# Performance work log

Measured on AMD Instinct MI355X. Metric: run time of the kernel, lower is better.

## Reference

```python
import jax, jax.numpy as jnp
import numpy as np

N_NODES = 100000
N_EDGES = 1600000
N_GRAPHS = 512
HIDDEN = 128
N_LAYERS = 3


def setup_inputs() -> dict:
    key = jax.random.key(0)
    ks = jax.random.split(key, 16)
    X = jax.random.normal(ks[0], (N_NODES, HIDDEN), dtype=jnp.float32)
    edge_index = jax.random.randint(ks[1], (2, N_EDGES), 0, N_NODES, dtype=jnp.int64)
    batch = jnp.sort(jax.random.randint(ks[2], (N_NODES,), 0, N_GRAPHS, dtype=jnp.int64))
    s = 1.0 / np.sqrt(HIDDEN)
    mlp_w1 = jax.random.normal(ks[3], (N_LAYERS, HIDDEN, HIDDEN), dtype=jnp.float32) * s
    mlp_b1 = jnp.zeros((N_LAYERS, HIDDEN), dtype=jnp.float32)
    mlp_w2 = jax.random.normal(ks[4], (N_LAYERS, HIDDEN, HIDDEN), dtype=jnp.float32) * s
    mlp_b2 = jnp.zeros((N_LAYERS, HIDDEN), dtype=jnp.float32)
    cls_w1 = jax.random.normal(ks[5], (HIDDEN * N_LAYERS, HIDDEN), dtype=jnp.float32) / np.sqrt(HIDDEN * N_LAYERS)
    cls_b1 = jnp.zeros((HIDDEN,), dtype=jnp.float32)
    cls_w2 = jax.random.normal(ks[6], (HIDDEN, HIDDEN), dtype=jnp.float32) * s
    cls_b2 = jnp.zeros((HIDDEN,), dtype=jnp.float32)
    cls_w3 = jax.random.normal(ks[7], (HIDDEN, 1), dtype=jnp.float32) * s
    cls_b3 = jnp.zeros((1,), dtype=jnp.float32)
    return {"X": X, "edge_index": edge_index, "batch": batch,
            "mlp_w1": mlp_w1, "mlp_b1": mlp_b1, "mlp_w2": mlp_w2, "mlp_b2": mlp_b2,
            "cls_w1": cls_w1, "cls_b1": cls_b1, "cls_w2": cls_w2, "cls_b2": cls_b2,
            "cls_w3": cls_w3, "cls_b3": cls_b3}


def reference(X, edge_index, batch, mlp_w1, mlp_b1, mlp_w2, mlp_b2,
              cls_w1, cls_b1, cls_w2, cls_b2, cls_w3, cls_b3):
    src, dst = edge_index[0], edge_index[1]
    xs = []
    for l in range(N_LAYERS):
        # GIN aggregation: sum_{j in N(i)} x_j ; eps = 0 so add self feature
        agg = jax.ops.segment_sum(X[src], dst, num_segments=N_NODES)  # [N, H]
        z = X + agg
        # 2-layer MLP update
        h = jax.nn.relu(z @ mlp_w1[l] + mlp_b1[l])
        h = h @ mlp_w2[l] + mlp_b2[l]
        # dropout is identity in eval; then relu
        X = jax.nn.relu(h)
        # global sum pooling per graph
        xs.append(jax.ops.segment_sum(X, batch, num_segments=N_GRAPHS))  # [G, H]
    h = jnp.concatenate(xs, axis=-1)  # JK 'cat' -> [G, H*L]
    h = jax.nn.relu(h @ cls_w1 + cls_b1)
    h = jax.nn.relu(h @ cls_w2 + cls_b2)
    logits = h @ cls_w3 + cls_b3  # [G, 1]
    return logits
```

## Files before the change

### kernel.cpp

```cpp
#include <hip/hip_runtime.h>
#include <hip/hip_fp16.h>
#include <cstddef>
#include <cstdint>

#define N_NODES   100000
#define N_EDGES   1600000
#define N_GRAPHS  512
#define HIDDEN    128
#define N_LAYERS  3

#define N_WIN        400
#define WIN_NODES    (N_NODES / N_WIN)
#define PLACE_BLOCKS 128
#define PCHUNK       (N_EDGES / PLACE_BLOCKS)

#define F2H_BLOCKS   ((N_NODES * HIDDEN / 8) / 256)
#define WCONV_BLOCKS (N_LAYERS * 2 * 16)
#define GB_BLOCKS    2
#define PREP_BLOCKS  (F2H_BLOCKS + WCONV_BLOCKS + GB_BLOCKS)

typedef _Float16 half8  __attribute__((ext_vector_type(8)));
typedef _Float16 half4v __attribute__((ext_vector_type(4)));
typedef _Float16 half2v __attribute__((ext_vector_type(2)));
typedef float    float8 __attribute__((ext_vector_type(8)));
typedef float    floatx4 __attribute__((ext_vector_type(4)));
typedef float    floatx2 __attribute__((ext_vector_type(2)));

__global__ __launch_bounds__(256) void win_count_kernel(const int* __restrict__ dst,
                                                        int* __restrict__ counts) {
    __shared__ int cs[N_WIN];
    for (int i = threadIdx.x; i < N_WIN; i += 256) cs[i] = 0;
    __syncthreads();
    const int4* d4 = (const int4*)(dst + blockIdx.x * PCHUNK);
    for (int i = threadIdx.x; i < PCHUNK / 4; i += 256) {
        int4 d = d4[i];
        atomicAdd(&cs[d.x / WIN_NODES], 1);
        atomicAdd(&cs[d.y / WIN_NODES], 1);
        atomicAdd(&cs[d.z / WIN_NODES], 1);
        atomicAdd(&cs[d.w / WIN_NODES], 1);
    }
    __syncthreads();
    for (int i = threadIdx.x; i < N_WIN; i += 256)
        counts[blockIdx.x * N_WIN + i] = cs[i];
}

__global__ __launch_bounds__(128) void win_scan1_kernel(const int* __restrict__ counts,
                                                        int* __restrict__ offsets,
                                                        int* __restrict__ colsum) {
    __shared__ int tmp[128];
    const int w = blockIdx.x;
    const int t = threadIdx.x;
    tmp[t] = counts[t * N_WIN + w];
    __syncthreads();
#pragma unroll
    for (int off = 1; off < 128; off <<= 1) {
        int u = (t >= off) ? tmp[t - off] : 0;
        __syncthreads();
        tmp[t] += u;
        __syncthreads();
    }
    offsets[t * N_WIN + w] = (t == 0) ? 0 : tmp[t - 1];
    if (t == 127) colsum[w] = tmp[127];
}

__global__ __launch_bounds__(512) void win_place_kernel(const int* __restrict__ src,
                                                        const int* __restrict__ dst,
                                                        const int* __restrict__ offsets,
                                                        const int* __restrict__ colsum,
                                                        int2* __restrict__ wedge) {
    __shared__ int ws[512];
    __shared__ int off[N_WIN];
    const int t = threadIdx.x;
    ws[t] = (t < N_WIN) ? colsum[t] : 0;
    __syncthreads();
#pragma unroll
    for (int o = 1; o < 512; o <<= 1) {
        int u = (t >= o) ? ws[t - o] : 0;
        __syncthreads();
        ws[t] += u;
        __syncthreads();
    }
    if (t < N_WIN) off[t] = offsets[blockIdx.x * N_WIN + t] + ((t == 0) ? 0 : ws[t - 1]);
    __syncthreads();
    const int4* d4 = (const int4*)(dst + blockIdx.x * PCHUNK);
    const int4* s4 = (const int4*)(src + blockIdx.x * PCHUNK);
    for (int i = t; i < PCHUNK / 4; i += 512) {
        int4 d = d4[i];
        int4 s = s4[i];
        int p0 = atomicAdd(&off[d.x / WIN_NODES], 1); wedge[p0] = make_int2(d.x, s.x);
        int p1 = atomicAdd(&off[d.y / WIN_NODES], 1); wedge[p1] = make_int2(d.y, s.y);
        int p2 = atomicAdd(&off[d.z / WIN_NODES], 1); wedge[p2] = make_int2(d.z, s.z);
        int p3 = atomicAdd(&off[d.w / WIN_NODES], 1); wedge[p3] = make_int2(d.w, s.w);
    }
}

__global__ __launch_bounds__(512) void win_csr_kernel(const int2* __restrict__ wedge,
                                                      const int* __restrict__ colsum,
                                                      int* __restrict__ row_ptr,
                                                      int* __restrict__ csr_src) {
    __shared__ int ws[512];
    __shared__ int cnt[WIN_NODES];
    __shared__ int bb[2];
    const int w = blockIdx.x, n0 = w * WIN_NODES, t = threadIdx.x;
    ws[t] = (t < N_WIN) ? colsum[t] : 0;
    __syncthreads();
#pragma unroll
    for (int o = 1; o < 512; o <<= 1) {
        int u = (t >= o) ? ws[t - o] : 0;
        __syncthreads();
        ws[t] += u;
        __syncthreads();
    }
    if (t == 0) { bb[0] = (w > 0) ? ws[w - 1] : 0; bb[1] = ws[w]; }
    if (w == N_WIN - 1 && t == 0) row_ptr[N_NODES] = ws[N_WIN - 1];
    for (int i = t; i < WIN_NODES; i += 512) cnt[i] = 0;
    __syncthreads();
    const int b0 = bb[0], b1 = bb[1];
    for (int e = b0 + t; e < b1; e += 512)
        atomicAdd(&cnt[wedge[e].x - n0], 1);
    __syncthreads();
    ws[t] = (t < WIN_NODES) ? cnt[t] : 0;
    __syncthreads();
#pragma unroll
    for (int o = 1; o < 512; o <<= 1) {
        int u = (t >= o) ? ws[t - o] : 0;
        __syncthreads();
        ws[t] += u;
        __syncthreads();
    }
    const int excl = (t == 0) ? 0 : ws[t - 1];
    if (t < WIN_NODES) {
        row_ptr[n0 + t] = b0 + excl;
        cnt[t] = b0 + excl;
    }
    __syncthreads();
    for (int e = b0 + t; e < b1; e += 512) {
        int2 ed = wedge[e];
        int p = atomicAdd(&cnt[ed.x - n0], 1);
        csr_src[p] = ed.y;
    }
}

__global__ __launch_bounds__(256) void prep_kernel(const float* __restrict__ X,
                                                   __half* __restrict__ hA,
                                                   unsigned char* __restrict__ outq,
                                                   const float* __restrict__ w1,
                                                   const float* __restrict__ w2,
                                                   __half* __restrict__ wt1,
                                                   __half* __restrict__ wt2,
                                                   const int* __restrict__ batch,
                                                   int* __restrict__ gstart) {
    __shared__ float tile[32][33];
    const int b = blockIdx.x;
    if (b < F2H_BLOCKS) {
        int t = b * 256 + threadIdx.x;
        const float4* in4 = (const float4*)X;
        float4 a = in4[t * 2 + 0];
        float4 c = in4[t * 2 + 1];
        __half2* o2 = (__half2*)hA;
        o2[t * 4 + 0] = __floats2half2_rn(a.x, a.y);
        o2[t * 4 + 1] = __floats2half2_rn(a.z, a.w);
        o2[t * 4 + 2] = __floats2half2_rn(c.x, c.y);
        o2[t * 4 + 3] = __floats2half2_rn(c.z, c.w);
        unsigned r0 = 0, r1 = 0;
        r0 = __builtin_amdgcn_cvt_pk_fp8_f32(a.x, a.y, r0, false);
        r0 = __builtin_amdgcn_cvt_pk_fp8_f32(a.z, a.w, r0, true);
        r1 = __builtin_amdgcn_cvt_pk_fp8_f32(c.x, c.y, r1, false);
        r1 = __builtin_amdgcn_cvt_pk_fp8_f32(c.z, c.w, r1, true);
        ((uint2*)outq)[t] = make_uint2(r0, r1);
    } else if (b < F2H_BLOCKS + WCONV_BLOCKS) {
        const int bb = b - F2H_BLOCKS;
        const int mat = bb & 1;
        const int tt = (bb >> 1) & 15;
        const int l  = bb >> 5;
        const int ti = (tt >> 2) * 32, tj = (tt & 3) * 32;
        const float* W = (mat ? w2 : w1) + (size_t)l * HIDDEN * HIDDEN;
        __half* WT = (mat ? wt2 : wt1) + (size_t)l * HIDDEN * HIDDEN;
        const int r = threadIdx.x >> 5;
        const int c = threadIdx.x & 31;
#pragma unroll
        for (int rr = 0; rr < 4; ++rr)
            tile[r + 8 * rr][c] = W[(size_t)(ti + r + 8 * rr) * HIDDEN + tj + c];
        __syncthreads();
#pragma unroll
        for (int rr = 0; rr < 4; ++rr)
            WT[(size_t)(tj + r + 8 * rr) * HIDDEN + ti + c] =
                __float2half(tile[c][r + 8 * rr]);
    } else {
        const int g = (b - F2H_BLOCKS - WCONV_BLOCKS) * 256 + threadIdx.x;
        if (g < N_GRAPHS) {
            int lo = 0, hi = N_NODES;
            while (lo < hi) {
                int mid = (lo + hi) >> 1;
                if (batch[mid] < g) lo = mid + 1; else hi = mid;
            }
            gstart[g] = lo;
        }
        if (g == 0) gstart[N_GRAPHS] = N_NODES;
    }
}

__device__ __forceinline__ void acc_fp8x16(float* acc, uint4 v) {
    floatx2 f;
    f = __builtin_amdgcn_cvt_pk_f32_fp8(v.x, false); acc[0] += f.x;  acc[1] += f.y;
    f = __builtin_amdgcn_cvt_pk_f32_fp8(v.x, true);  acc[2] += f.x;  acc[3] += f.y;
    f = __builtin_amdgcn_cvt_pk_f32_fp8(v.y, false); acc[4] += f.x;  acc[5] += f.y;
    f = __builtin_amdgcn_cvt_pk_f32_fp8(v.y, true);  acc[6] += f.x;  acc[7] += f.y;
    f = __builtin_amdgcn_cvt_pk_f32_fp8(v.z, false); acc[8] += f.x;  acc[9] += f.y;
    f = __builtin_amdgcn_cvt_pk_f32_fp8(v.z, true);  acc[10] += f.x; acc[11] += f.y;
    f = __builtin_amdgcn_cvt_pk_f32_fp8(v.w, false); acc[12] += f.x; acc[13] += f.y;
    f = __builtin_amdgcn_cvt_pk_f32_fp8(v.w, true);  acc[14] += f.x; acc[15] += f.y;
}

__device__ __forceinline__ void gather_body(int wave, int lane,
                                            const unsigned char* __restrict__ Xq,
                                            const __half* __restrict__ Xh,
                                            __half* __restrict__ Zh,
                                            const int* __restrict__ row_ptr,
                                            const int* __restrict__ csr_src) {
    const int grp = lane >> 3;
    const int m   = lane & 7;
    const uint4* Q = (const uint4*)Xq;

    float acc[16];
#pragma unroll
    for (int j = 0; j < 16; ++j) acc[j] = 0.f;

    int k = row_ptr[wave];
    const int end = row_ptr[wave + 1];

    for (; k + 16 <= end; k += 16) {
        int n0 = csr_src[k + grp];
        int n1 = csr_src[k + 8 + grp];
        uint4 v0 = Q[(size_t)n0 * 8 + m];
        uint4 v1 = Q[(size_t)n1 * 8 + m];
        acc_fp8x16(acc, v0);
        acc_fp8x16(acc, v1);
    }
    if (k + 8 <= end) {
        int n0 = csr_src[k + grp];
        uint4 v0 = Q[(size_t)n0 * 8 + m];
        acc_fp8x16(acc, v0);
        k += 8;
    }
    int rem = end - k;
    if (grp < rem) {
        int n0 = csr_src[k + grp];
        uint4 v0 = Q[(size_t)n0 * 8 + m];
        acc_fp8x16(acc, v0);
    }

    half2v hh[8];
#pragma unroll
    for (int j = 0; j < 8; ++j) {
        hh[j][0] = (_Float16)acc[2 * j];
        hh[j][1] = (_Float16)acc[2 * j + 1];
    }
#pragma unroll
    for (int j = 0; j < 8; ++j) {
        int b = __shfl_xor(__builtin_bit_cast(int, hh[j]), 8);
        hh[j] = hh[j] + __builtin_bit_cast(half2v, b);
    }
#pragma unroll
    for (int j = 0; j < 8; ++j) {
        int b = __shfl_xor(__builtin_bit_cast(int, hh[j]), 16);
        hh[j] = hh[j] + __builtin_bit_cast(half2v, b);
    }
#pragma unroll
    for (int j = 0; j < 8; ++j) {
        int b = __shfl_xor(__builtin_bit_cast(int, hh[j]), 32);
        hh[j] = hh[j] + __builtin_bit_cast(half2v, b);
    }

    if (grp == 0) {
        const half2v* H2 = (const half2v*)(Xh + (size_t)wave * HIDDEN + 16 * m);
        half8 o0, o1;
#pragma unroll
        for (int j = 0; j < 4; ++j) {
            half2v s = hh[j] + H2[j];
            o0[2 * j] = s[0]; o0[2 * j + 1] = s[1];
        }
#pragma unroll
        for (int j = 0; j < 4; ++j) {
            half2v s = hh[4 + j] + H2[4 + j];
            o1[2 * j] = s[0]; o1[2 * j + 1] = s[1];
        }
        ((half8*)(Zh + (size_t)wave * HIDDEN + 16 * m))[0] = o0;
        ((half8*)(Zh + (size_t)wave * HIDDEN + 16 * m))[1] = o1;
    }
}

__global__ void gather_kernel(const unsigned char* __restrict__ Xq,
                              const __half* __restrict__ Xh,
                              __half* __restrict__ Zh,
                              const int* __restrict__ row_ptr,
                              const int* __restrict__ csr_src) {
    int wave = (blockIdx.x * blockDim.x + threadIdx.x) >> 6;
    if (wave >= N_NODES) return;
    gather_body(wave, threadIdx.x & 63, Xq, Xh, Zh, row_ptr, csr_src);
}

__device__ __forceinline__ void gpool_body(int g,
                                           const __half* __restrict__ Xh,
                                           const int* __restrict__ gstart,
                                           float* __restrict__ pooled, int layer) {
    __shared__ float red[16][16][8];
    const int f8 = threadIdx.x & 15;
    const int qt = threadIdx.x >> 4;
    const int s = gstart[g], e = gstart[g + 1];

    float acc[8];
#pragma unroll
    for (int j = 0; j < 8; ++j) acc[j] = 0.f;

    for (int n = s + qt; n < e; n += 16) {
        half8 v = ((const half8*)(Xh + (size_t)n * HIDDEN))[f8];
#pragma unroll
        for (int j = 0; j < 8; ++j) acc[j] += (float)v[j];
    }
#pragma unroll
    for (int j = 0; j < 8; ++j) red[qt][f8][j] = acc[j];
    __syncthreads();

    if (threadIdx.x < 128) {
        const int c = threadIdx.x;
        float sum = 0.f;
#pragma unroll
        for (int p = 0; p < 16; ++p) sum += red[p][c >> 3][c & 7];
        pooled[(size_t)g * (HIDDEN * N_LAYERS) + layer * HIDDEN + c] = sum;
    }
}

__global__ __launch_bounds__(256) void gpool_kernel(const __half* __restrict__ Xh,
                                                    const int* __restrict__ gstart,
                                                    float* __restrict__ pooled,
                                                    int layer) {
    gpool_body(blockIdx.x, Xh, gstart, pooled, layer);
}

#define POOL_BLKS N_GRAPHS
__global__ __launch_bounds__(256) void gather_pool_kernel(const unsigned char* __restrict__ Xq,
                                                          const __half* __restrict__ Xh,
                                                          __half* __restrict__ Zh,
                                                          const int* __restrict__ row_ptr,
                                                          const int* __restrict__ csr_src,
                                                          const int* __restrict__ gstart,
                                                          float* __restrict__ pooled,
                                                          int prev_layer) {
    if (blockIdx.x < POOL_BLKS) {
        gpool_body(blockIdx.x, Xh, gstart, pooled, prev_layer);
        return;
    }
    int wave = ((blockIdx.x - POOL_BLKS) * 256 + threadIdx.x) >> 6;
    if (wave >= N_NODES) return;
    gather_body(wave, threadIdx.x & 63, Xq, Xh, Zh, row_ptr, csr_src);
}

#define MM_BLOCKS 1024
__global__ __launch_bounds__(256) void mm_ws_kernel(const __half* __restrict__ A,
                                                    const __half* __restrict__ Wt,
                                                    const float* __restrict__ bias,
                                                    __half* __restrict__ C16,
                                                    unsigned char* __restrict__ Q8) {
    const int tid  = threadIdx.x;
    const int wid  = tid >> 6;
    const int lane = tid & 63;
    const int m    = lane & 15;
    const int q    = lane >> 4;
    const int NTILES = N_NODES / 16;

    half8 wf[2][4];
    float bl[2][4];
#pragma unroll
    for (int s = 0; s < 2; ++s) {
        const int ct = 2 * wid + s;
        const half8* Wrow = (const half8*)(Wt + (size_t)(ct * 16 + m) * HIDDEN);
#pragma unroll
        for (int c = 0; c < 4; ++c) wf[s][c] = Wrow[c * 4 + q];
#pragma unroll
        for (int r = 0; r < 4; ++r) bl[s][r] = bias[ct * 16 + q * 4 + r];
    }

    int t = blockIdx.x;
    half8 a0, a1, a2, a3;
    {
        const half8* Arow = (const half8*)(A + (size_t)(t * 16 + m) * HIDDEN);
        a0 = Arow[q]; a1 = Arow[4 + q]; a2 = Arow[8 + q]; a3 = Arow[12 + q];
    }

    while (true) {
        const int tn = t + MM_BLOCKS;
        half8 n0, n1, n2, n3;
        if (tn < NTILES) {
            const half8* Nrow = (const half8*)(A + (size_t)(tn * 16 + m) * HIDDEN);
            n0 = Nrow[q]; n1 = Nrow[4 + q]; n2 = Nrow[8 + q]; n3 = Nrow[12 + q];
        }

        __half* Cr = C16 + (size_t)(t * 16 + m) * HIDDEN + q * 4;
#pragma unroll
        for (int s = 0; s < 2; ++s) {
            const int ct = 2 * wid + s;
            floatx4 acc = {0.f, 0.f, 0.f, 0.f};
            acc = __builtin_amdgcn_mfma_f32_16x16x32_f16(wf[s][0], a0, acc, 0, 0, 0);
            acc = __builtin_amdgcn_mfma_f32_16x16x32_f16(wf[s][1], a1, acc, 0, 0, 0);
            acc = __builtin_amdgcn_mfma_f32_16x16x32_f16(wf[s][2], a2, acc, 0, 0, 0);
            acc = __builtin_amdgcn_mfma_f32_16x16x32_f16(wf[s][3], a3, acc, 0, 0, 0);
            float v0 = fmaxf(acc[0] + bl[s][0], 0.f);
            float v1 = fmaxf(acc[1] + bl[s][1], 0.f);
            float v2 = fmaxf(acc[2] + bl[s][2], 0.f);
            float v3 = fmaxf(acc[3] + bl[s][3], 0.f);
            half4v o;
            o[0] = (_Float16)v0; o[1] = (_Float16)v1;
            o[2] = (_Float16)v2; o[3] = (_Float16)v3;
            *(half4v*)(Cr + ct * 16) = o;
            if (Q8) {
                unsigned r0 = 0;
                r0 = __builtin_amdgcn_cvt_pk_fp8_f32(v0, v1, r0, false);
                r0 = __builtin_amdgcn_cvt_pk_fp8_f32(v2, v3, r0, true);
                *(unsigned*)(Q8 + (size_t)(t * 16 + m) * HIDDEN + ct * 16 + q * 4) = r0;
            }
        }

        if (tn >= NTILES) break;
        t = tn;
        a0 = n0; a1 = n1; a2 = n2; a3 = n3;
    }
}

__global__ __launch_bounds__(128) void cls_kernel(const float* __restrict__ pooled,
                                                  const float* __restrict__ w1,
                                                  const float* __restrict__ b1,
                                                  const float* __restrict__ w2,
                                                  const float* __restrict__ b2,
                                                  const float* __restrict__ w3,
                                                  const float* __restrict__ b3,
                                                  float* __restrict__ out) {
    __shared__ float hin[HIDDEN * N_LAYERS];
    __shared__ float h1[HIDDEN];
    __shared__ float red[HIDDEN];
    const int g = blockIdx.x;
    const int t = threadIdx.x;

    for (int i = t; i < HIDDEN * N_LAYERS; i += 128)
        hin[i] = pooled[(size_t)g * (HIDDEN * N_LAYERS) + i];
    __syncthreads();

    float s = 0.f;
    for (int k = 0; k < HIDDEN * N_LAYERS; ++k) s += hin[k] * w1[(size_t)k * HIDDEN + t];
    s = fmaxf(s + b1[t], 0.f);
    h1[t] = s;
    __syncthreads();

    float s2 = 0.f;
    for (int k = 0; k < HIDDEN; ++k) s2 += h1[k] * w2[(size_t)k * HIDDEN + t];
    s2 = fmaxf(s2 + b2[t], 0.f);

    red[t] = s2 * w3[t];
    __syncthreads();
    for (int off = 64; off > 0; off >>= 1) {
        if (t < off) red[t] += red[t + off];
        __syncthreads();
    }
    if (t == 0) out[g] = red[0] + b3[0];
}

extern "C" void kernel_launch(void* const* d_in, const int* in_sizes, int n_in,
                              void* d_out, int out_size, void* d_ws, size_t ws_size,
                              hipStream_t stream) {
    const float* X     = (const float*)d_in[0];
    const int*   ei    = (const int*)d_in[1];
    const int*   batch = (const int*)d_in[2];
    const float* w1all = (const float*)d_in[3];
    const float* b1all = (const float*)d_in[4];
    const float* w2all = (const float*)d_in[5];
    const float* b2all = (const float*)d_in[6];
    const float* cw1   = (const float*)d_in[7];
    const float* cb1   = (const float*)d_in[8];
    const float* cw2   = (const float*)d_in[9];
    const float* cb2   = (const float*)d_in[10];
    const float* cw3   = (const float*)d_in[11];
    const float* cb3   = (const float*)d_in[12];
    float* out = (float*)d_out;

    const int* src = ei;
    const int* dst = ei + N_EDGES;

    char* p = (char*)d_ws;
    auto alloc2 = [&](size_t bytes) {
        char* r = p;
        p += (bytes + 255) & ~(size_t)255;
        return r;
    };
    __half* hA      = (__half*)alloc2((size_t)N_NODES * HIDDEN * sizeof(__half));
    __half* hB      = (__half*)alloc2((size_t)N_NODES * HIDDEN * sizeof(__half));
    __half* zh      = (__half*)alloc2((size_t)N_NODES * HIDDEN * sizeof(__half));
    __half* m1h     = (__half*)alloc2((size_t)N_NODES * HIDDEN * sizeof(__half));
    unsigned char* qbuf = (unsigned char*)alloc2((size_t)N_NODES * HIDDEN);
    __half* wt1     = (__half*)alloc2((size_t)N_LAYERS * HIDDEN * HIDDEN * sizeof(__half));
    __half* wt2     = (__half*)alloc2((size_t)N_LAYERS * HIDDEN * HIDDEN * sizeof(__half));
    int2*   wedge   = (int2*)alloc2((size_t)N_EDGES * sizeof(int2));
    int*    csr     = (int*)alloc2((size_t)N_EDGES * sizeof(int));
    int*    rowp    = (int*)alloc2((size_t)(N_NODES + 1) * sizeof(int));
    int*    counts  = (int*)alloc2((size_t)PLACE_BLOCKS * N_WIN * sizeof(int));
    int*    offsets = (int*)alloc2((size_t)PLACE_BLOCKS * N_WIN * sizeof(int));
    int*    colsum  = (int*)alloc2((size_t)N_WIN * sizeof(int));
    int*    gstart  = (int*)alloc2((size_t)(N_GRAPHS + 1) * sizeof(int));
    float*  pooled  = (float*)alloc2((size_t)N_GRAPHS * HIDDEN * N_LAYERS * sizeof(float));

    win_count_kernel<<<PLACE_BLOCKS, 256, 0, stream>>>(dst, counts);
    win_scan1_kernel<<<N_WIN, 128, 0, stream>>>(counts, offsets, colsum);
    win_place_kernel<<<PLACE_BLOCKS, 512, 0, stream>>>(src, dst, offsets, colsum, wedge);
    win_csr_kernel<<<N_WIN, 512, 0, stream>>>(wedge, colsum, rowp, csr);

    prep_kernel<<<PREP_BLOCKS, 256, 0, stream>>>(X, hA, qbuf, w1all, w2all, wt1, wt2,
                                                 batch, gstart);

    const int gat_grid = (N_NODES + 3) / 4;

    __half* hcur = hA;
    for (int l = 0; l < N_LAYERS; ++l) {
        __half* hnext = (l & 1) ? hA : hB;
        const bool emit = (l < N_LAYERS - 1);
        if (l == 0) {
            gather_kernel<<<gat_grid, 256, 0, stream>>>(qbuf, hcur, zh, rowp, csr);
        } else {
            gather_pool_kernel<<<gat_grid + POOL_BLKS, 256, 0, stream>>>(
                qbuf, hcur, zh, rowp, csr, gstart, pooled, l - 1);
        }
        mm_ws_kernel<<<MM_BLOCKS, 256, 0, stream>>>(zh,
                                                    wt1 + (size_t)l * HIDDEN * HIDDEN,
                                                    b1all + (size_t)l * HIDDEN,
                                                    m1h, (unsigned char*)nullptr);
        mm_ws_kernel<<<MM_BLOCKS, 256, 0, stream>>>(m1h,
                                                    wt2 + (size_t)l * HIDDEN * HIDDEN,
                                                    b2all + (size_t)l * HIDDEN,
                                                    hnext,
                                                    emit ? qbuf : (unsigned char*)nullptr);
        hcur = hnext;
    }

    gpool_kernel<<<N_GRAPHS, 256, 0, stream>>>(hcur, gstart, pooled, N_LAYERS - 1);
    cls_kernel<<<N_GRAPHS, 128, 0, stream>>>(pooled, cw1, cb1, cw2, cb2, cw3, cb3, out);
}
```

Measured before the change: 462.5 us.

## Fuse both MLP matmuls into one kernel with LDS-staged hidden tile

Replaces the two per-layer matmul launches with one fused kernel. Each 512-thread block computes the first 16x128 GEMM tile, writes the ReLU output into a swizzled, double-buffered LDS tile, synchronises, and runs the second GEMM from LDS. This removes the intermediate m1h global round trip (write and reread of 100k x 128 fp16 per layer) and one launch per layer. In exchange it adds a block-wide barrier per tile and drops the previous next-tile register prefetch.

```diff
diff --git a/kernel.cpp b/kernel.cpp
--- a/kernel.cpp
+++ b/kernel.cpp
@@ -356,74 +356,91 @@
     gather_body(wave, threadIdx.x & 63, Xq, Xh, Zh, row_ptr, csr_src);
 }
 
-#define MM_BLOCKS 1024
-__global__ __launch_bounds__(256) void mm_ws_kernel(const __half* __restrict__ A,
-                                                    const __half* __restrict__ Wt,
-                                                    const float* __restrict__ bias,
-                                                    __half* __restrict__ C16,
-                                                    unsigned char* __restrict__ Q8) {
+#define MMF_BLOCKS 2048
+__global__ __launch_bounds__(512) void mlp_ws_kernel(const __half* __restrict__ A,
+                                                     const __half* __restrict__ Wt1,
+                                                     const __half* __restrict__ Wt2,
+                                                     const float* __restrict__ b1,
+                                                     const float* __restrict__ b2,
+                                                     __half* __restrict__ C16,
+                                                     unsigned char* __restrict__ Q8) {
+    __shared__ _Float16 hs[2][16][128];
+
     const int tid  = threadIdx.x;
-    const int wid  = tid >> 6;
+    const int wv   = tid >> 6;
     const int lane = tid & 63;
     const int m    = lane & 15;
     const int q    = lane >> 4;
     const int NTILES = N_NODES / 16;
 
-    half8 wf[2][4];
-    float bl[2][4];
-#pragma unroll
-    for (int s = 0; s < 2; ++s) {
-        const int ct = 2 * wid + s;
-        const half8* Wrow = (const half8*)(Wt + (size_t)(ct * 16 + m) * HIDDEN);
-#pragma unroll
-        for (int c = 0; c < 4; ++c) wf[s][c] = Wrow[c * 4 + q];
-#pragma unroll
-        for (int r = 0; r < 4; ++r) bl[s][r] = bias[ct * 16 + q * 4 + r];
-    }
-
-    int t = blockIdx.x;
-    half8 a0, a1, a2, a3;
+    half8 wf1[4], wf2[4];
+    float bl1[4], bl2[4];
     {
+        const half8* W1row = (const half8*)(Wt1 + (size_t)(wv * 16 + m) * HIDDEN);
+        const half8* W2row = (const half8*)(Wt2 + (size_t)(wv * 16 + m) * HIDDEN);
+#pragma unroll
+        for (int c = 0; c < 4; ++c) { wf1[c] = W1row[c * 4 + q]; wf2[c] = W2row[c * 4 + q]; }
+#pragma unroll
+        for (int r = 0; r < 4; ++r) {
+            bl1[r] = b1[wv * 16 + q * 4 + r];
+            bl2[r] = b2[wv * 16 + q * 4 + r];
+        }
+    }
+
+    _Float16* hwr0 = &hs[0][m][(((2 * wv + (q >> 1)) ^ m) << 3) + ((q & 1) << 2)];
+    _Float16* hwr1 = &hs[1][m][(((2 * wv + (q >> 1)) ^ m) << 3) + ((q & 1) << 2)];
+    const _Float16* hrd0 = &hs[0][m][0];
+    const _Float16* hrd1 = &hs[1][m][0];
+
+    int buf = 0;
+    for (int t = blockIdx.x; t < NTILES; t += MMF_BLOCKS) {
         const half8* Arow = (const half8*)(A + (size_t)(t * 16 + m) * HIDDEN);
-        a0 = Arow[q]; a1 = Arow[4 + q]; a2 = Arow[8 + q]; a3 = Arow[12 + q];
-    }
-
-    while (true) {
-        const int tn = t + MM_BLOCKS;
-        half8 n0, n1, n2, n3;
-        if (tn < NTILES) {
-            const half8* Nrow = (const half8*)(A + (size_t)(tn * 16 + m) * HIDDEN);
-            n0 = Nrow[q]; n1 = Nrow[4 + q]; n2 = Nrow[8 + q]; n3 = Nrow[12 + q];
-        }
-
-        __half* Cr = C16 + (size_t)(t * 16 + m) * HIDDEN + q * 4;
-#pragma unroll
-        for (int s = 0; s < 2; ++s) {
-            const int ct = 2 * wid + s;
+        half8 a0 = Arow[q];
+        half8 a1 = Arow[4 + q];
+        half8 a2 = Arow[8 + q];
+        half8 a3 = Arow[12 + q];
+
+        {
             floatx4 acc = {0.f, 0.f, 0.f, 0.f};
-            acc = __builtin_amdgcn_mfma_f32_16x16x32_f16(wf[s][0], a0, acc, 0, 0, 0);
-            acc = __builtin_amdgcn_mfma_f32_16x16x32_f16(wf[s][1], a1, acc, 0, 0, 0);
-            acc = __builtin_amdgcn_mfma_f32_16x16x32_f16(wf[s][2], a2, acc, 0, 0, 0);
-            acc = __builtin_amdgcn_mfma_f32_16x16x32_f16(wf[s][3], a3, acc, 0, 0, 0);
-            float v0 = fmaxf(acc[0] + bl[s][0], 0.f);
-            float v1 = fmaxf(acc[1] + bl[s][1], 0.f);
-            float v2 = fmaxf(acc[2] + bl[s][2], 0.f);
-            float v3 = fmaxf(acc[3] + bl[s][3], 0.f);
+            acc = __builtin_amdgcn_mfma_f32_16x16x32_f16(wf1[0], a0, acc, 0, 0, 0);
+            acc = __builtin_amdgcn_mfma_f32_16x16x32_f16(wf1[1], a1, acc, 0, 0, 0);
+            acc = __builtin_amdgcn_mfma_f32_16x16x32_f16(wf1[2], a2, acc, 0, 0, 0);
+            acc = __builtin_amdgcn_mfma_f32_16x16x32_f16(wf1[3], a3, acc, 0, 0, 0);
+            half4v o;
+#pragma unroll
+            for (int r = 0; r < 4; ++r) o[r] = (_Float16)fmaxf(acc[r] + bl1[r], 0.f);
+            *(half4v*)(buf ? hwr1 : hwr0) = o;
+        }
+        __syncthreads();
+
+        {
+            const _Float16* hr = buf ? hrd1 : hrd0;
+            half8 h0 = *(const half8*)(hr + (((0 + q) ^ m) << 3));
+            half8 h1 = *(const half8*)(hr + (((4 + q) ^ m) << 3));
+            half8 h2 = *(const half8*)(hr + (((8 + q) ^ m) << 3));
+            half8 h3 = *(const half8*)(hr + (((12 + q) ^ m) << 3));
+            floatx4 acc = {0.f, 0.f, 0.f, 0.f};
+            acc = __builtin_amdgcn_mfma_f32_16x16x32_f16(wf2[0], h0, acc, 0, 0, 0);
+            acc = __builtin_amdgcn_mfma_f32_16x16x32_f16(wf2[1], h1, acc, 0, 0, 0);
+            acc = __builtin_amdgcn_mfma_f32_16x16x32_f16(wf2[2], h2, acc, 0, 0, 0);
+            acc = __builtin_amdgcn_mfma_f32_16x16x32_f16(wf2[3], h3, acc, 0, 0, 0);
+            float v0 = fmaxf(acc[0] + bl2[0], 0.f);
+            float v1 = fmaxf(acc[1] + bl2[1], 0.f);
+            float v2 = fmaxf(acc[2] + bl2[2], 0.f);
+            float v3 = fmaxf(acc[3] + bl2[3], 0.f);
+            const size_t base = (size_t)(t * 16 + m) * HIDDEN + wv * 16 + q * 4;
             half4v o;
             o[0] = (_Float16)v0; o[1] = (_Float16)v1;
             o[2] = (_Float16)v2; o[3] = (_Float16)v3;
-            *(half4v*)(Cr + ct * 16) = o;
+            *(half4v*)(C16 + base) = o;
             if (Q8) {
                 unsigned r0 = 0;
                 r0 = __builtin_amdgcn_cvt_pk_fp8_f32(v0, v1, r0, false);
                 r0 = __builtin_amdgcn_cvt_pk_fp8_f32(v2, v3, r0, true);
-                *(unsigned*)(Q8 + (size_t)(t * 16 + m) * HIDDEN + ct * 16 + q * 4) = r0;
+                *(unsigned*)(Q8 + base) = r0;
             }
         }
-
-        if (tn >= NTILES) break;
-        t = tn;
-        a0 = n0; a1 = n1; a2 = n2; a3 = n3;
+        buf ^= 1;
     }
 }
 
@@ -494,7 +511,6 @@
     __half* hA      = (__half*)alloc2((size_t)N_NODES * HIDDEN * sizeof(__half));
     __half* hB      = (__half*)alloc2((size_t)N_NODES * HIDDEN * sizeof(__half));
     __half* zh      = (__half*)alloc2((size_t)N_NODES * HIDDEN * sizeof(__half));
-    __half* m1h     = (__half*)alloc2((size_t)N_NODES * HIDDEN * sizeof(__half));
     unsigned char* qbuf = (unsigned char*)alloc2((size_t)N_NODES * HIDDEN);
     __half* wt1     = (__half*)alloc2((size_t)N_LAYERS * HIDDEN * HIDDEN * sizeof(__half));
     __half* wt2     = (__half*)alloc2((size_t)N_LAYERS * HIDDEN * HIDDEN * sizeof(__half));
@@ -527,15 +543,13 @@
             gather_pool_kernel<<<gat_grid + POOL_BLKS, 256, 0, stream>>>(
                 qbuf, hcur, zh, rowp, csr, gstart, pooled, l - 1);
         }
-        mm_ws_kernel<<<MM_BLOCKS, 256, 0, stream>>>(zh,
-                                                    wt1 + (size_t)l * HIDDEN * HIDDEN,
-                                                    b1all + (size_t)l * HIDDEN,
-                                                    m1h, (unsigned char*)nullptr);
-        mm_ws_kernel<<<MM_BLOCKS, 256, 0, stream>>>(m1h,
-                                                    wt2 + (size_t)l * HIDDEN * HIDDEN,
-                                                    b2all + (size_t)l * HIDDEN,
-                                                    hnext,
-                                                    emit ? qbuf : (unsigned char*)nullptr);
+        mlp_ws_kernel<<<MMF_BLOCKS, 512, 0, stream>>>(zh,
+                                                      wt1 + (size_t)l * HIDDEN * HIDDEN,
+                                                      wt2 + (size_t)l * HIDDEN * HIDDEN,
+                                                      b1all + (size_t)l * HIDDEN,
+                                                      b2all + (size_t)l * HIDDEN,
+                                                      hnext,
+                                                      emit ? qbuf : (unsigned char*)nullptr);
         hcur = hnext;
     }
 
```

New measurement: 461.8 us. About the same (-0.1%).
